# Optimization experiments

Hardware: AMD Instinct MI355X
Metric: run time of the kernel (lower is better)

The kernel has to match this reference:

```python
import jax, jax.numpy as jnp
import numpy as np

B, C_IN, C_OUT, H, W, K = 8, 32, 32, 96, 96, 5


def setup_inputs() -> dict:
    key = jax.random.key(0)
    k1, k2 = jax.random.split(key)
    f = jax.random.normal(k1, (B, C_IN, H, W), dtype=jnp.float32)
    # xavier_uniform-style init for the structuring element h
    fan_in = C_IN * K * K
    fan_out = C_OUT * K * K
    bound = float(np.sqrt(6.0 / (fan_in + fan_out)))
    h = jax.random.uniform(k2, (C_OUT, C_IN, K, K), dtype=jnp.float32,
                           minval=-bound, maxval=bound)
    return {"f": f, "h": h}


def reference(f, h):
    """Morphological max-plus dilation with 'same' padding.

    out[b,o,y,x] = max_{c,i,j} f[b,c,y+i-p, x+j-p] + h[o,c,i,j]
    """
    b, c, hh, ww = f.shape
    o, _, k, _ = h.shape
    p = k // 2
    neg = -jnp.finfo(f.dtype).max / 2
    fp = jnp.pad(f, ((0, 0), (0, 0), (p, p), (p, p)), constant_values=neg)
    out = jnp.full((b, o, hh, ww), neg, dtype=f.dtype)
    for i in range(k):          # fixed small kernel loop (k*k = 25 taps)
        for j in range(k):
            sl = fp[:, :, i:i + hh, j:j + ww]              # (B, C, H, W)
            w_ij = h[:, :, i, j]                            # (O, C)
            # max-plus over input channels: (B,1,C,H,W) + (O,C,1,1)
            cand = jnp.max(sl[:, None] + w_ij[None, :, :, None, None], axis=2)
            out = jnp.maximum(out, cand)
    return out
```

## Files before the change

kernel.cpp:

```cpp
#include <hip/hip_runtime.h>
#include <hip/hip_fp16.h>


#define B_ 8
#define C_ 32
#define O_ 32
#define H_ 96
#define W_ 96
#define K_ 5

#define TX_ 24
#define TY_ 8
#define NT_ (TX_ * TY_)
#define XR_ 4
#define OP_ 2
#define OB_ (OP_ * 2)

#define PH_ 100
#define PW_ 104

#define NEGF (-30000.0f)

typedef _Float16 h2 __attribute__((ext_vector_type(2)));

static __device__ __forceinline__ h2 h2_from_bits(unsigned u) {
    return __builtin_bit_cast(h2, u);
}
static __device__ __forceinline__ unsigned bits_from_h2(h2 v) {
    return __builtin_bit_cast(unsigned, v);
}

__global__ __launch_bounds__(256)
void prepad_kernel(const float* __restrict__ f, unsigned* __restrict__ fpad) {
    const int idx = blockIdx.x * 256 + threadIdx.x;
    const int c = blockIdx.y;
    const int b = blockIdx.z;
    if (idx >= PH_ * PW_) return;
    const int row = idx / PW_;
    const int col = idx - row * PW_;
    const int y = row - 2;
    const int x = col - 2;
    float v = NEGF;
    if ((unsigned)y < H_ && (unsigned)x < W_)
        v = f[((size_t)(b * C_ + c) * H_ + y) * W_ + x];
    _Float16 hv = (_Float16)v;
    h2 d; d.x = hv; d.y = hv;
    fpad[((size_t)(b * C_ + c) * PH_ + row) * PW_ + col] = bits_from_h2(d);
}

template <bool PADDED>
__global__ __launch_bounds__(NT_)
void dilate_main(const unsigned* __restrict__ fpad, const float* __restrict__ f,
                 const float* __restrict__ h, float* __restrict__ out) {
    const int tx  = threadIdx.x;
    const int ty  = threadIdx.y;
    const int tid = ty * TX_ + tx;

    const int ytile = blockIdx.x;
    const int og    = blockIdx.y;
    const int b     = blockIdx.z;
    const int y0 = ytile * TY_;
    const int o0 = og * OB_;
    const int x0 = XR_ * tx;

    __shared__ unsigned hs[C_][K_][K_][OP_];
    for (int idx = tid; idx < C_ * K_ * K_ * OP_; idx += NT_) {
        int c  = idx / (K_ * K_ * OP_);
        int r  = idx - c * (K_ * K_ * OP_);
        int ij = r / OP_;
        int op = r - ij * OP_;
        int o  = o0 + 2 * op;
        float h0 = h[((size_t)o * C_ + c) * (K_ * K_) + ij];
        float h1 = h[((size_t)(o + 1) * C_ + c) * (K_ * K_) + ij];
        h2 p; p.x = (_Float16)h0; p.y = (_Float16)h1;
        hs[c][ij / K_][ij - (ij / K_) * K_][op] = bits_from_h2(p);
    }
    __syncthreads();

    h2 acc[OP_][XR_];
    {
        h2 neg; neg.x = (_Float16)NEGF; neg.y = (_Float16)NEGF;
#pragma unroll
        for (int op = 0; op < OP_; ++op)
#pragma unroll
            for (int xx = 0; xx < XR_; ++xx) acc[op][xx] = neg;
    }

    for (int c = 0; c < C_; ++c) {
        h2 a[K_][8];
        if (PADDED) {
            const unsigned* fp = fpad + (size_t)(b * C_ + c) * (PH_ * PW_);
#pragma unroll
            for (int i = 0; i < K_; ++i) {
                const int row = y0 + ty + i;
                const uint4* p = (const uint4*)(fp + row * PW_ + 4 * tx);
                uint4 w0 = p[0];
                uint4 w1 = p[1];
                a[i][0] = h2_from_bits(w0.x); a[i][1] = h2_from_bits(w0.y);
                a[i][2] = h2_from_bits(w0.z); a[i][3] = h2_from_bits(w0.w);
                a[i][4] = h2_from_bits(w1.x); a[i][5] = h2_from_bits(w1.y);
                a[i][6] = h2_from_bits(w1.z); a[i][7] = h2_from_bits(w1.w);
            }
        } else {
            const float* fc = f + (size_t)(b * C_ + c) * (H_ * W_);
#pragma unroll
            for (int i = 0; i < K_; ++i) {
                const int yy = y0 + ty + i - 2;
                const bool yok = (unsigned)yy < H_;
                const float* frow = fc + (size_t)(yok ? yy : 0) * W_;
#pragma unroll
                for (int t = 0; t < 8; ++t) {
                    int xc = x0 - 2 + t;
                    bool ok = yok && ((unsigned)xc < W_);
                    float v = frow[ok ? xc : 0];
                    v = ok ? v : NEGF;
                    _Float16 hv = (_Float16)v;
                    h2 d; d.x = hv; d.y = hv;
                    a[i][t] = d;
                }
            }
        }

#pragma unroll
        for (int i = 0; i < K_; ++i) {
#pragma unroll
            for (int j = 0; j < K_; ++j) {
                uint2 hb = *(const uint2*)&hs[c][i][j][0];
                h2 h0 = h2_from_bits(hb.x);
                h2 h1 = h2_from_bits(hb.y);
#pragma unroll
                for (int xx = 0; xx < XR_; ++xx) {
                    h2 fv = a[i][xx + j];
                    acc[0][xx] = __builtin_elementwise_max(acc[0][xx], fv + h0);
                    acc[1][xx] = __builtin_elementwise_max(acc[1][xx], fv + h1);
                }
            }
        }
    }

    const int y = y0 + ty;
#pragma unroll
    for (int op = 0; op < OP_; ++op) {
        const int o = o0 + 2 * op;
        float4 lo = make_float4((float)acc[op][0].x, (float)acc[op][1].x,
                                (float)acc[op][2].x, (float)acc[op][3].x);
        float4 hi = make_float4((float)acc[op][0].y, (float)acc[op][1].y,
                                (float)acc[op][2].y, (float)acc[op][3].y);
        *(float4*)&out[(((size_t)b * O_ + o)     * H_ + y) * W_ + x0] = lo;
        *(float4*)&out[(((size_t)b * O_ + o + 1) * H_ + y) * W_ + x0] = hi;
    }
}

extern "C" void kernel_launch(void* const* d_in, const int* in_sizes, int n_in,
                              void* d_out, int out_size, void* d_ws, size_t ws_size,
                              hipStream_t stream) {
    const float* f = (const float*)d_in[0];
    const float* h = (const float*)d_in[1];
    float* out = (float*)d_out;

    dim3 mgrid(H_ / TY_, O_ / OB_, B_);
    dim3 mblock(TX_, TY_);

    const size_t need = (size_t)B_ * C_ * PH_ * PW_ * sizeof(unsigned);
    if (ws_size >= need) {
        unsigned* fpad = (unsigned*)d_ws;
        dim3 pgrid((PH_ * PW_ + 255) / 256, C_, B_);
        hipLaunchKernelGGL(prepad_kernel, pgrid, dim3(256), 0, stream, f, fpad);
        hipLaunchKernelGGL((dilate_main<true>), mgrid, mblock, 0, stream,
                           fpad, f, h, out);
    } else {
        hipLaunchKernelGGL((dilate_main<false>), mgrid, mblock, 0, stream,
                           (const unsigned*)nullptr, f, h, out);
    }
}
```

Before: 158.4 us.

## Split input channels across two thread groups and reduce via shared memory

Each block now holds two groups of 192 threads. Each group handles half the input channels for the same output tile, so every thread runs a serial loop of 16 channels instead of 32. The second group writes its partial max accumulators to shared memory, and the first group combines them and stores the result. This shortens the per-thread critical path and doubles the threads per block at the same grid size, at the cost of a barrier, an extra LDS exchange, and half the threads sitting idle during the epilogue.

Result: faster. 146.7 us (-7.4%).

```diff
diff --git a/kernel.cpp b/kernel.cpp
--- a/kernel.cpp
+++ b/kernel.cpp
@@ -10,11 +10,14 @@
 #define K_ 5
 
 #define TX_ 24
-#define TY_ 8
+#define RY_ 8
+#define CS_ 2
+#define TY_ (RY_ * CS_)
 #define NT_ (TX_ * TY_)
 #define XR_ 4
 #define OP_ 2
 #define OB_ (OP_ * 2)
+#define CG_ (C_ / CS_)
 
 #define PH_ 100
 #define PW_ 104
@@ -55,20 +58,24 @@
     const int tx  = threadIdx.x;
     const int ty  = threadIdx.y;
     const int tid = ty * TX_ + tx;
+    const int g   = ty >> 3;
+    const int r   = ty & 7;
+    const int t192 = r * TX_ + tx;
 
     const int ytile = blockIdx.x;
     const int og    = blockIdx.y;
     const int b     = blockIdx.z;
-    const int y0 = ytile * TY_;
+    const int y0 = ytile * RY_;
     const int o0 = og * OB_;
     const int x0 = XR_ * tx;
 
     __shared__ unsigned hs[C_][K_][K_][OP_];
+    __shared__ unsigned comb[OP_ * XR_][RY_ * TX_];
     for (int idx = tid; idx < C_ * K_ * K_ * OP_; idx += NT_) {
         int c  = idx / (K_ * K_ * OP_);
-        int r  = idx - c * (K_ * K_ * OP_);
-        int ij = r / OP_;
-        int op = r - ij * OP_;
+        int rr = idx - c * (K_ * K_ * OP_);
+        int ij = rr / OP_;
+        int op = rr - ij * OP_;
         int o  = o0 + 2 * op;
         float h0 = h[((size_t)o * C_ + c) * (K_ * K_) + ij];
         float h1 = h[((size_t)(o + 1) * C_ + c) * (K_ * K_) + ij];
@@ -86,13 +93,15 @@
             for (int xx = 0; xx < XR_; ++xx) acc[op][xx] = neg;
     }
 
-    for (int c = 0; c < C_; ++c) {
+    const int cbase = g * CG_;
+    for (int cc = 0; cc < CG_; ++cc) {
+        const int c = cbase + cc;
         h2 a[K_][8];
         if (PADDED) {
             const unsigned* fp = fpad + (size_t)(b * C_ + c) * (PH_ * PW_);
 #pragma unroll
             for (int i = 0; i < K_; ++i) {
-                const int row = y0 + ty + i;
+                const int row = y0 + r + i;
                 const uint4* p = (const uint4*)(fp + row * PW_ + 4 * tx);
                 uint4 w0 = p[0];
                 uint4 w1 = p[1];
@@ -105,7 +114,7 @@
             const float* fc = f + (size_t)(b * C_ + c) * (H_ * W_);
 #pragma unroll
             for (int i = 0; i < K_; ++i) {
-                const int yy = y0 + ty + i - 2;
+                const int yy = y0 + r + i - 2;
                 const bool yok = (unsigned)yy < H_;
                 const float* frow = fc + (size_t)(yok ? yy : 0) * W_;
 #pragma unroll
@@ -138,16 +147,34 @@
         }
     }
 
-    const int y = y0 + ty;
-#pragma unroll
-    for (int op = 0; op < OP_; ++op) {
-        const int o = o0 + 2 * op;
-        float4 lo = make_float4((float)acc[op][0].x, (float)acc[op][1].x,
-                                (float)acc[op][2].x, (float)acc[op][3].x);
-        float4 hi = make_float4((float)acc[op][0].y, (float)acc[op][1].y,
-                                (float)acc[op][2].y, (float)acc[op][3].y);
-        *(float4*)&out[(((size_t)b * O_ + o)     * H_ + y) * W_ + x0] = lo;
-        *(float4*)&out[(((size_t)b * O_ + o + 1) * H_ + y) * W_ + x0] = hi;
+    if (g == 1) {
+#pragma unroll
+        for (int op = 0; op < OP_; ++op)
+#pragma unroll
+            for (int xx = 0; xx < XR_; ++xx)
+                comb[op * XR_ + xx][t192] = bits_from_h2(acc[op][xx]);
+    }
+    __syncthreads();
+    if (g == 0) {
+#pragma unroll
+        for (int op = 0; op < OP_; ++op)
+#pragma unroll
+            for (int xx = 0; xx < XR_; ++xx) {
+                h2 other = h2_from_bits(comb[op * XR_ + xx][t192]);
+                acc[op][xx] = __builtin_elementwise_max(acc[op][xx], other);
+            }
+
+        const int y = y0 + r;
+#pragma unroll
+        for (int op = 0; op < OP_; ++op) {
+            const int o = o0 + 2 * op;
+            float4 lo = make_float4((float)acc[op][0].x, (float)acc[op][1].x,
+                                    (float)acc[op][2].x, (float)acc[op][3].x);
+            float4 hi = make_float4((float)acc[op][0].y, (float)acc[op][1].y,
+                                    (float)acc[op][2].y, (float)acc[op][3].y);
+            *(float4*)&out[(((size_t)b * O_ + o)     * H_ + y) * W_ + x0] = lo;
+            *(float4*)&out[(((size_t)b * O_ + o + 1) * H_ + y) * W_ + x0] = hi;
+        }
     }
 }
 
@@ -158,7 +185,7 @@
     const float* h = (const float*)d_in[1];
     float* out = (float*)d_out;
 
-    dim3 mgrid(H_ / TY_, O_ / OB_, B_);
+    dim3 mgrid(H_ / RY_, O_ / OB_, B_);
     dim3 mblock(TX_, TY_);
 
     const size_t need = (size_t)B_ * C_ * PH_ * PW_ * sizeof(unsigned);
```
